# Kernel tuning notes

Hardware: AMD Instinct MI355X
Metric: run time of the kernel (lower is better)

## Reference

```python
import jax, jax.numpy as jnp
import numpy as np


def setup_inputs() -> dict:
    key = jax.random.key(0)
    k1, k2 = jax.random.split(key)
    B, Lc, Lm, D = 8, 2048, 2048, 128
    context = jax.random.normal(k1, (B, Lc, D), dtype=jnp.float32)
    main = jax.random.normal(k2, (B, Lm, D), dtype=jnp.float32)
    return {"context": context, "main": main}


def reference(context, main):
    # weights[b,c,m] = sum_d context[b,c,d] * main[b,m,d]   (Keras dot axes=[2,2])
    weights = jnp.einsum("bcd,bmd->bcm", context, main)
    # K.softmax default axis=-1: normalize over the main-length axis m
    weights = jax.nn.softmax(weights, axis=-1)
    # dot([weights, context], axes=1): contract axis 1 (c) of both -> (B, Lm, D)
    weighted = jnp.einsum("bcm,bcd->bmd", weights, context)
    return main - weighted
```

## Files before the change

### kernel.cpp

```cpp
#include <hip/hip_runtime.h>


#define BATCH 8
#define L_SEQ 2048
#define DD 128
#define SHIFT 40.0f
#define LDA 136
#define ESLD 72

typedef __attribute__((ext_vector_type(8))) short bf16x8;
typedef __attribute__((ext_vector_type(4))) float f32x4;

__device__ __forceinline__ short f2bf(float f) {
    unsigned u = __builtin_bit_cast(unsigned, f);
    return (short)((u + 0x8000u) >> 16);
}

template <int NT>
__device__ __forceinline__ void stage_tile(short* __restrict__ dst,
                                           const float* __restrict__ src,
                                           int nelts, int t) {
    for (int base = 0; base < nelts; base += NT * 8) {
        int flat = base + t * 8;
        const float4* p = (const float4*)(src + flat);
        float4 v0 = p[0];
        float4 v1 = p[1];
        bf16x8 s;
        s[0] = f2bf(v0.x); s[1] = f2bf(v0.y); s[2] = f2bf(v0.z); s[3] = f2bf(v0.w);
        s[4] = f2bf(v1.x); s[5] = f2bf(v1.y); s[6] = f2bf(v1.z); s[7] = f2bf(v1.w);
        int row = flat >> 7;
        int col = flat & 127;
        *(bf16x8*)&dst[row * LDA + col] = s;
    }
}

__global__ __launch_bounds__(256) void zero_kernel(float* __restrict__ p, int n) {
    int i = blockIdx.x * 256 + threadIdx.x;
    if (i < n) p[i] = 0.0f;
}


__global__ __launch_bounds__(256, 4) void stats_kernel(const float* __restrict__ ctx,
                                                       const float* __restrict__ mn,
                                                       float* __restrict__ Lg,
                                                       short* __restrict__ Eg) {
    __shared__ short Cs[64 * LDA];
    __shared__ short Ms[64 * LDA];
    __shared__ short Es[64 * ESLD];

    int bid = blockIdx.x;
    int mc = bid & 3;
    int ct = (bid >> 2) & 31;
    int b  = bid >> 7;
    int t = threadIdx.x;
    int w = t >> 6;
    int l = t & 63;
    int a15 = l & 15;
    int q = l >> 4;

    stage_tile<256>(Cs, ctx + ((size_t)b * L_SEQ + ct * 64) * DD, 64 * DD, t);

    float ls[4] = {0.f, 0.f, 0.f, 0.f};

    for (int mt = 0; mt < 8; ++mt) {
        __syncthreads();
        int m0 = (mc * 8 + mt) * 64;
        stage_tile<256>(Ms, mn + ((size_t)b * L_SEQ + m0) * DD, 64 * DD, t);
        __syncthreads();

        f32x4 sacc[4] = {{0.f,0.f,0.f,0.f},{0.f,0.f,0.f,0.f},{0.f,0.f,0.f,0.f},{0.f,0.f,0.f,0.f}};
        #pragma unroll
        for (int ks = 0; ks < 4; ++ks) {
            int k0 = ks * 32 + q * 8;
            bf16x8 a = *(const bf16x8*)&Ms[(w * 16 + a15) * LDA + k0];
            #pragma unroll
            for (int cg = 0; cg < 4; ++cg) {
                bf16x8 bb = *(const bf16x8*)&Cs[(cg * 16 + a15) * LDA + k0];
                sacc[cg] = __builtin_amdgcn_mfma_f32_16x16x32_bf16(a, bb, sacc[cg], 0, 0, 0);
            }
        }
        #pragma unroll
        for (int cg = 0; cg < 4; ++cg) {
            #pragma unroll
            for (int r = 0; r < 4; ++r) {
                float e = __expf(sacc[cg][r] - SHIFT);
                ls[cg] += e;
                Es[(w * 16 + q * 4 + r) * ESLD + cg * 16 + a15] = f2bf(e);
            }
        }
        __syncthreads();
        #pragma unroll
        for (int i = 0; i < 2; ++i) {
            int flat = i * 2048 + t * 8;
            int m = flat >> 6;
            int c = flat & 63;
            bf16x8 v = *(const bf16x8*)&Es[m * ESLD + c];
            *(bf16x8*)&Eg[((size_t)b * L_SEQ + m0 + m) * L_SEQ + ct * 64 + c] = v;
        }
    }

    #pragma unroll
    for (int cg = 0; cg < 4; ++cg) {
        float v = ls[cg];
        v += __shfl_xor(v, 16);
        v += __shfl_xor(v, 32);
        ls[cg] = v;
    }
    if (l < 16) {
        #pragma unroll
        for (int cg = 0; cg < 4; ++cg)
            atomicAdd(&Lg[(size_t)b * L_SEQ + ct * 64 + cg * 16 + l], ls[cg]);
    }
}

__global__ __launch_bounds__(256) void prep_kernel(const float* __restrict__ ctx,
                                                   const float* __restrict__ Lg,
                                                   short* __restrict__ CtL) {
    __shared__ short Ts[128 * LDA];
    __shared__ float invLs[128];

    int b = blockIdx.x >> 4;
    int cc = blockIdx.x & 15;
    int t = threadIdx.x;

    if (t < 128) invLs[t] = 1.0f / Lg[(size_t)b * L_SEQ + cc * 128 + t];
    __syncthreads();

    const float* src = ctx + ((size_t)b * L_SEQ + cc * 128) * DD;
    #pragma unroll
    for (int i = 0; i < 8; ++i) {
        int flat = i * 2048 + t * 8;
        int r = flat >> 7;
        int c = flat & 127;
        const float4* p = (const float4*)(src + flat);
        float4 v0 = p[0];
        float4 v1 = p[1];
        float il = invLs[r];
        bf16x8 s;
        s[0] = f2bf(v0.x * il); s[1] = f2bf(v0.y * il); s[2] = f2bf(v0.z * il); s[3] = f2bf(v0.w * il);
        s[4] = f2bf(v1.x * il); s[5] = f2bf(v1.y * il); s[6] = f2bf(v1.z * il); s[7] = f2bf(v1.w * il);
        *(bf16x8*)&Ts[r * LDA + c] = s;
    }
    __syncthreads();

    int d = t >> 1;
    int ch = (t & 1) * 64;
    #pragma unroll
    for (int i = 0; i < 8; ++i) {
        int c = ch + i * 8;
        bf16x8 v;
        #pragma unroll
        for (int j = 0; j < 8; ++j) v[j] = Ts[(c + j) * LDA + d];
        *(bf16x8*)&CtL[((size_t)b * DD + d) * L_SEQ + cc * 128 + c] = v;
    }
}

__global__ __launch_bounds__(256, 4) void attend_kernel(const short* __restrict__ Eg,
                                                        const short* __restrict__ CtL,
                                                        const float* __restrict__ mn,
                                                        float* __restrict__ out) {
    __shared__ short Ct[128 * LDA];
    __shared__ short Et[32 * LDA];

    int bid = blockIdx.x;
    int mtile = bid & 63;
    int b = bid >> 6;
    int m0 = mtile * 32;
    int t = threadIdx.x;
    int w = t >> 6;
    int l = t & 63;
    int a15 = l & 15;
    int q = l >> 4;

    f32x4 oacc[2][2] = {{{0.f,0.f,0.f,0.f},{0.f,0.f,0.f,0.f}},
                        {{0.f,0.f,0.f,0.f},{0.f,0.f,0.f,0.f}}};

    for (int cs = 0; cs < 16; ++cs) {
        int c0 = cs * 128;
        __syncthreads();
        #pragma unroll
        for (int i = 0; i < 8; ++i) {
            int flat = i * 2048 + t * 8;
            int d = flat >> 7;
            int c = flat & 127;
            bf16x8 v = *(const bf16x8*)&CtL[((size_t)b * DD + d) * L_SEQ + c0 + c];
            *(bf16x8*)&Ct[d * LDA + c] = v;
        }
        #pragma unroll
        for (int i = 0; i < 2; ++i) {
            int flat = i * 2048 + t * 8;
            int m = flat >> 7;
            int c = flat & 127;
            bf16x8 v = *(const bf16x8*)&Eg[((size_t)b * L_SEQ + m0 + m) * L_SEQ + c0 + c];
            *(bf16x8*)&Et[m * LDA + c] = v;
        }
        __syncthreads();

        #pragma unroll
        for (int ks = 0; ks < 4; ++ks) {
            int k0 = ks * 32 + q * 8;
            bf16x8 a0 = *(const bf16x8*)&Et[a15 * LDA + k0];
            bf16x8 a1 = *(const bf16x8*)&Et[(16 + a15) * LDA + k0];
            #pragma unroll
            for (int g = 0; g < 2; ++g) {
                bf16x8 bb = *(const bf16x8*)&Ct[((w * 2 + g) * 16 + a15) * LDA + k0];
                oacc[0][g] = __builtin_amdgcn_mfma_f32_16x16x32_bf16(a0, bb, oacc[0][g], 0, 0, 0);
                oacc[1][g] = __builtin_amdgcn_mfma_f32_16x16x32_bf16(a1, bb, oacc[1][g], 0, 0, 0);
            }
        }
    }

    #pragma unroll
    for (int mg = 0; mg < 2; ++mg) {
        #pragma unroll
        for (int g = 0; g < 2; ++g) {
            int d = (w * 2 + g) * 16 + a15;
            #pragma unroll
            for (int r = 0; r < 4; ++r) {
                int m = m0 + mg * 16 + q * 4 + r;
                size_t idx = ((size_t)b * L_SEQ + m) * DD + d;
                out[idx] = mn[idx] - oacc[mg][g][r];
            }
        }
    }
}


__global__ __launch_bounds__(256, 4) void stats_fb(const float* __restrict__ ctx,
                                                   const float* __restrict__ mn,
                                                   float* __restrict__ Lg) {
    __shared__ short Cs[64 * LDA];
    __shared__ short Ms[64 * LDA];

    int bid = blockIdx.x;
    int mc = bid & 3;
    int ct = (bid >> 2) & 31;
    int b  = bid >> 7;
    int t = threadIdx.x;
    int w = t >> 6;
    int l = t & 63;
    int a15 = l & 15;
    int q = l >> 4;

    stage_tile<256>(Cs, ctx + ((size_t)b * L_SEQ + ct * 64) * DD, 64 * DD, t);

    float ls[4] = {0.f, 0.f, 0.f, 0.f};
    for (int mt = 0; mt < 8; ++mt) {
        __syncthreads();
        int m0 = (mc * 8 + mt) * 64;
        stage_tile<256>(Ms, mn + ((size_t)b * L_SEQ + m0) * DD, 64 * DD, t);
        __syncthreads();

        f32x4 acc[4] = {{0.f,0.f,0.f,0.f},{0.f,0.f,0.f,0.f},{0.f,0.f,0.f,0.f},{0.f,0.f,0.f,0.f}};
        #pragma unroll
        for (int ks = 0; ks < 4; ++ks) {
            int k0 = ks * 32 + q * 8;
            bf16x8 a = *(const bf16x8*)&Cs[(w * 16 + a15) * LDA + k0];
            #pragma unroll
            for (int g = 0; g < 4; ++g) {
                bf16x8 bb = *(const bf16x8*)&Ms[(g * 16 + a15) * LDA + k0];
                acc[g] = __builtin_amdgcn_mfma_f32_16x16x32_bf16(a, bb, acc[g], 0, 0, 0);
            }
        }
        #pragma unroll
        for (int g = 0; g < 4; ++g)
            #pragma unroll
            for (int r = 0; r < 4; ++r)
                ls[r] += __expf(acc[g][r] - SHIFT);
    }

    #pragma unroll
    for (int r = 0; r < 4; ++r) {
        float v = ls[r];
        v += __shfl_xor(v, 1);
        v += __shfl_xor(v, 2);
        v += __shfl_xor(v, 4);
        v += __shfl_xor(v, 8);
        ls[r] = v;
    }
    if (a15 == 0) {
        int c = ct * 64 + w * 16 + q * 4;
        #pragma unroll
        for (int r = 0; r < 4; ++r)
            atomicAdd(&Lg[(size_t)b * L_SEQ + c + r], ls[r]);
    }
}

__global__ __launch_bounds__(1024, 4) void attend_fb(const float* __restrict__ ctx,
                                                     const float* __restrict__ mn,
                                                     const float* __restrict__ Lg,
                                                     float* __restrict__ out) {
    __shared__ short Mt[64 * LDA];
    __shared__ short Cs[128 * LDA];
    __shared__ short Ct[128 * LDA];
    __shared__ short Ps[64 * LDA];
    __shared__ float invLs[128];

    int bid = blockIdx.x;
    int mtile = bid & 31;
    int b = bid >> 5;
    int m0 = mtile * 64;
    int t = threadIdx.x;
    int w = t >> 6;
    int l = t & 63;
    int a15 = l & 15;
    int q = l >> 4;
    int mg = w & 3;
    int pg = w >> 2;

    stage_tile<1024>(Mt, mn + ((size_t)b * L_SEQ + m0) * DD, 64 * DD, t);

    f32x4 oacc[2] = {{0.f,0.f,0.f,0.f},{0.f,0.f,0.f,0.f}};

    for (int cs = 0; cs < 16; ++cs) {
        int c0 = cs * 128;
        __syncthreads();
        stage_tile<1024>(Cs, ctx + ((size_t)b * L_SEQ + c0) * DD, 128 * DD, t);
        if (t < 128) invLs[t] = 1.0f / Lg[(size_t)b * L_SEQ + c0 + t];
        __syncthreads();

        {
            int cc = t & 127;
            int d0 = (t >> 7) * 16;
            #pragma unroll
            for (int h = 0; h < 2; ++h) {
                bf16x8 v = *(const bf16x8*)&Cs[cc * LDA + d0 + h * 8];
                #pragma unroll
                for (int j = 0; j < 8; ++j)
                    Ct[(d0 + h * 8 + j) * LDA + cc] = v[j];
            }
        }

        f32x4 sacc[2] = {{0.f,0.f,0.f,0.f},{0.f,0.f,0.f,0.f}};
        #pragma unroll
        for (int ks = 0; ks < 4; ++ks) {
            int k0 = ks * 32 + q * 8;
            bf16x8 a = *(const bf16x8*)&Mt[(mg * 16 + a15) * LDA + k0];
            #pragma unroll
            for (int g = 0; g < 2; ++g) {
                bf16x8 bb = *(const bf16x8*)&Cs[((pg * 2 + g) * 16 + a15) * LDA + k0];
                sacc[g] = __builtin_amdgcn_mfma_f32_16x16x32_bf16(a, bb, sacc[g], 0, 0, 0);
            }
        }
        #pragma unroll
        for (int g = 0; g < 2; ++g) {
            int cl = (pg * 2 + g) * 16 + a15;
            float il = invLs[cl];
            #pragma unroll
            for (int r = 0; r < 4; ++r) {
                float p = __expf(sacc[g][r] - SHIFT) * il;
                Ps[(mg * 16 + q * 4 + r) * LDA + cl] = f2bf(p);
            }
        }
        __syncthreads();

        #pragma unroll
        for (int ks = 0; ks < 4; ++ks) {
            int k0 = ks * 32 + q * 8;
            bf16x8 a = *(const bf16x8*)&Ps[(mg * 16 + a15) * LDA + k0];
            #pragma unroll
            for (int g = 0; g < 2; ++g) {
                bf16x8 bb = *(const bf16x8*)&Ct[((pg * 2 + g) * 16 + a15) * LDA + k0];
                oacc[g] = __builtin_amdgcn_mfma_f32_16x16x32_bf16(a, bb, oacc[g], 0, 0, 0);
            }
        }
    }

    #pragma unroll
    for (int g = 0; g < 2; ++g) {
        int dl = (pg * 2 + g) * 16 + a15;
        #pragma unroll
        for (int r = 0; r < 4; ++r) {
            int ml = mg * 16 + q * 4 + r;
            size_t idx = ((size_t)b * L_SEQ + m0 + ml) * DD + dl;
            out[idx] = mn[idx] - oacc[g][r];
        }
    }
}


extern "C" void kernel_launch(void* const* d_in, const int* in_sizes, int n_in,
                              void* d_out, int out_size, void* d_ws, size_t ws_size,
                              hipStream_t stream) {
    const float* ctx = (const float*)d_in[0];
    const float* mn  = (const float*)d_in[1];
    float* out = (float*)d_out;

    const size_t LG_BYTES  = (size_t)BATCH * L_SEQ * sizeof(float);
    const size_t CTL_BYTES = (size_t)BATCH * DD * L_SEQ * sizeof(short);
    const size_t E_BYTES   = (size_t)BATCH * L_SEQ * L_SEQ * sizeof(short);
    const size_t NEED = LG_BYTES + CTL_BYTES + E_BYTES;

    float* Lg = (float*)d_ws;
    int nL = BATCH * L_SEQ;
    zero_kernel<<<(nL + 255) / 256, 256, 0, stream>>>(Lg, nL);

    if (ws_size >= NEED) {
        short* CtL = (short*)((char*)d_ws + LG_BYTES);
        short* Eg  = (short*)((char*)d_ws + LG_BYTES + CTL_BYTES);
        stats_kernel<<<BATCH * 32 * 4, 256, 0, stream>>>(ctx, mn, Lg, Eg);
        prep_kernel<<<BATCH * 16, 256, 0, stream>>>(ctx, Lg, CtL);
        attend_kernel<<<BATCH * 64, 256, 0, stream>>>(Eg, CtL, mn, out);
    } else {
        stats_fb<<<BATCH * 32 * 4, 256, 0, stream>>>(ctx, mn, Lg);
        attend_fb<<<BATCH * 32, 1024, 0, stream>>>(ctx, mn, Lg, out);
    }
}
```

Measured before the change: 127.0 us.

## Pre-convert inputs to swizzled bf16 and stage tiles via direct global-to-LDS loads

Adds a convert kernel that writes context and main as XOR-swizzled bf16 copies and also zeroes the row-sum buffer, which removes the separate zero kernel. The stats and attend kernels then stage tiles with global_load_lds straight into unpadded, swizzled LDS. Attend double-buffers its E and C^T tiles so the next chunk loads while the current one is multiplied. The aim is to cut fp32 conversion work and register round-trips during staging and to hide global latency, at the cost of an extra pass over the inputs, more workspace and lower occupancy.

```diff
diff --git a/kernel.cpp b/kernel.cpp
--- a/kernel.cpp
+++ b/kernel.cpp
@@ -6,14 +6,21 @@
 #define DD 128
 #define SHIFT 40.0f
 #define LDA 136
-#define ESLD 72
+#define ESLD 80
 
 typedef __attribute__((ext_vector_type(8))) short bf16x8;
+typedef __attribute__((ext_vector_type(4))) short bf16x4;
 typedef __attribute__((ext_vector_type(4))) float f32x4;
 
 __device__ __forceinline__ short f2bf(float f) {
     unsigned u = __builtin_bit_cast(unsigned, f);
     return (short)((u + 0x8000u) >> 16);
+}
+
+__device__ __forceinline__ void gl2lds16(const short* g, short* l) {
+    __builtin_amdgcn_global_load_lds(
+        (const __attribute__((address_space(1))) unsigned int*)g,
+        (__attribute__((address_space(3))) unsigned int*)l, 16, 0, 0);
 }
 
 template <int NT>
@@ -40,12 +47,37 @@
 }
 
 
-__global__ __launch_bounds__(256, 4) void stats_kernel(const float* __restrict__ ctx,
-                                                       const float* __restrict__ mn,
+__global__ __launch_bounds__(256) void convert_kernel(const float* __restrict__ ctx,
+                                                      const float* __restrict__ mn,
+                                                      short* __restrict__ Cbf,
+                                                      short* __restrict__ Mbf,
+                                                      float* __restrict__ Lg) {
+    int tid = blockIdx.x * 256 + threadIdx.x;
+    if (tid < BATCH * L_SEQ) Lg[tid] = 0.0f;
+    const int half = BATCH * L_SEQ * DD / 8;
+    int id = tid;
+    const float* src;
+    short* dst;
+    if (id < half) { src = ctx; dst = Cbf; }
+    else           { id -= half; src = mn; dst = Mbf; }
+    int row = id >> 4;
+    int lc = id & 15;
+    const float4* p = (const float4*)(src + ((size_t)row << 7) + lc * 8);
+    float4 v0 = p[0];
+    float4 v1 = p[1];
+    bf16x8 s;
+    s[0] = f2bf(v0.x); s[1] = f2bf(v0.y); s[2] = f2bf(v0.z); s[3] = f2bf(v0.w);
+    s[4] = f2bf(v1.x); s[5] = f2bf(v1.y); s[6] = f2bf(v1.z); s[7] = f2bf(v1.w);
+    int pc = (lc & 8) | ((lc ^ row) & 7);
+    *(bf16x8*)&dst[((size_t)row << 7) + pc * 8] = s;
+}
+
+__global__ __launch_bounds__(256, 3) void stats_kernel(const short* __restrict__ Cbf,
+                                                       const short* __restrict__ Mbf,
                                                        float* __restrict__ Lg,
                                                        short* __restrict__ Eg) {
-    __shared__ short Cs[64 * LDA];
-    __shared__ short Ms[64 * LDA];
+    __shared__ short Cs[64 * 128];
+    __shared__ short Ms[64 * 128];
     __shared__ short Es[64 * ESLD];
 
     int bid = blockIdx.x;
@@ -57,59 +89,82 @@
     int l = t & 63;
     int a15 = l & 15;
     int q = l >> 4;
-
-    stage_tile<256>(Cs, ctx + ((size_t)b * L_SEQ + ct * 64) * DD, 64 * DD, t);
+    int h = a15 & 7;
+
+    {
+        const short* gC = Cbf + ((size_t)(b * L_SEQ + ct * 64)) * DD;
+        const short* gM = Mbf + ((size_t)(b * L_SEQ + mc * 512)) * DD;
+        #pragma unroll
+        for (int ii = 0; ii < 4; ++ii) {
+            int inst = w * 4 + ii;
+            gl2lds16(gC + inst * 512 + l * 8, Cs + inst * 512);
+            gl2lds16(gM + inst * 512 + l * 8, Ms + inst * 512);
+        }
+    }
 
     float ls[4] = {0.f, 0.f, 0.f, 0.f};
 
     for (int mt = 0; mt < 8; ++mt) {
-        __syncthreads();
-        int m0 = (mc * 8 + mt) * 64;
-        stage_tile<256>(Ms, mn + ((size_t)b * L_SEQ + m0) * DD, 64 * DD, t);
+        int m0 = mc * 512 + mt * 64;
         __syncthreads();
 
         f32x4 sacc[4] = {{0.f,0.f,0.f,0.f},{0.f,0.f,0.f,0.f},{0.f,0.f,0.f,0.f},{0.f,0.f,0.f,0.f}};
         #pragma unroll
         for (int ks = 0; ks < 4; ++ks) {
-            int k0 = ks * 32 + q * 8;
-            bf16x8 a = *(const bf16x8*)&Ms[(w * 16 + a15) * LDA + k0];
-            #pragma unroll
-            for (int cg = 0; cg < 4; ++cg) {
-                bf16x8 bb = *(const bf16x8*)&Cs[(cg * 16 + a15) * LDA + k0];
-                sacc[cg] = __builtin_amdgcn_mfma_f32_16x16x32_bf16(a, bb, sacc[cg], 0, 0, 0);
-            }
-        }
-        #pragma unroll
-        for (int cg = 0; cg < 4; ++cg) {
+            int aoff = ((ks * 4 + q) ^ h) * 8;
+            bf16x8 a = *(const bf16x8*)&Cs[(w * 16 + a15) * 128 + aoff];
+            #pragma unroll
+            for (int g = 0; g < 4; ++g) {
+                bf16x8 bb = *(const bf16x8*)&Ms[(g * 16 + a15) * 128 + aoff];
+                sacc[g] = __builtin_amdgcn_mfma_f32_16x16x32_bf16(a, bb, sacc[g], 0, 0, 0);
+            }
+        }
+        #pragma unroll
+        for (int g = 0; g < 4; ++g) {
+            bf16x4 pk;
             #pragma unroll
             for (int r = 0; r < 4; ++r) {
-                float e = __expf(sacc[cg][r] - SHIFT);
-                ls[cg] += e;
-                Es[(w * 16 + q * 4 + r) * ESLD + cg * 16 + a15] = f2bf(e);
-            }
-        }
-        __syncthreads();
+                float e = __expf(sacc[g][r] - SHIFT);
+                ls[r] += e;
+                pk[r] = f2bf(e);
+            }
+            *(bf16x4*)&Es[(g * 16 + a15) * ESLD + w * 16 + q * 4] = pk;
+        }
+        __syncthreads();
+
+        if (mt < 7) {
+            const short* gM = Mbf + ((size_t)(b * L_SEQ + m0 + 64)) * DD;
+            #pragma unroll
+            for (int ii = 0; ii < 4; ++ii) {
+                int inst = w * 4 + ii;
+                gl2lds16(gM + inst * 512 + l * 8, Ms + inst * 512);
+            }
+        }
         #pragma unroll
         for (int i = 0; i < 2; ++i) {
             int flat = i * 2048 + t * 8;
-            int m = flat >> 6;
-            int c = flat & 63;
-            bf16x8 v = *(const bf16x8*)&Es[m * ESLD + c];
-            *(bf16x8*)&Eg[((size_t)b * L_SEQ + m0 + m) * L_SEQ + ct * 64 + c] = v;
-        }
-    }
-
-    #pragma unroll
-    for (int cg = 0; cg < 4; ++cg) {
-        float v = ls[cg];
-        v += __shfl_xor(v, 16);
-        v += __shfl_xor(v, 32);
-        ls[cg] = v;
-    }
-    if (l < 16) {
-        #pragma unroll
-        for (int cg = 0; cg < 4; ++cg)
-            atomicAdd(&Lg[(size_t)b * L_SEQ + ct * 64 + cg * 16 + l], ls[cg]);
+            int ml = flat >> 6;
+            int cl = flat & 63;
+            bf16x8 v = *(const bf16x8*)&Es[ml * ESLD + cl];
+            int pcr = (cl >> 3) ^ (ml & 7);
+            *(bf16x8*)&Eg[((size_t)(b * L_SEQ + m0 + ml)) * L_SEQ + ct * 64 + pcr * 8] = v;
+        }
+    }
+
+    #pragma unroll
+    for (int r = 0; r < 4; ++r) {
+        float v = ls[r];
+        v += __shfl_xor(v, 1);
+        v += __shfl_xor(v, 2);
+        v += __shfl_xor(v, 4);
+        v += __shfl_xor(v, 8);
+        ls[r] = v;
+    }
+    if (a15 == 0) {
+        int c = ct * 64 + w * 16 + q * 4;
+        #pragma unroll
+        for (int r = 0; r < 4; ++r)
+            atomicAdd(&Lg[(size_t)b * L_SEQ + c + r], ls[r]);
     }
 }
 
@@ -126,7 +181,7 @@
     if (t < 128) invLs[t] = 1.0f / Lg[(size_t)b * L_SEQ + cc * 128 + t];
     __syncthreads();
 
-    const float* src = ctx + ((size_t)b * L_SEQ + cc * 128) * DD;
+    const float* src = ctx + ((size_t)(b * L_SEQ + cc * 128)) * DD;
     #pragma unroll
     for (int i = 0; i < 8; ++i) {
         int flat = i * 2048 + t * 8;
@@ -145,22 +200,24 @@
 
     int d = t >> 1;
     int ch = (t & 1) * 64;
+    int key = d & 7;
     #pragma unroll
     for (int i = 0; i < 8; ++i) {
         int c = ch + i * 8;
         bf16x8 v;
         #pragma unroll
         for (int j = 0; j < 8; ++j) v[j] = Ts[(c + j) * LDA + d];
-        *(bf16x8*)&CtL[((size_t)b * DD + d) * L_SEQ + cc * 128 + c] = v;
-    }
-}
-
-__global__ __launch_bounds__(256, 4) void attend_kernel(const short* __restrict__ Eg,
+        int pc = cc * 16 + (ch >> 3) + (i ^ key);
+        *(bf16x8*)&CtL[((size_t)(b * DD + d)) * L_SEQ + pc * 8] = v;
+    }
+}
+
+__global__ __launch_bounds__(256, 2) void attend_kernel(const short* __restrict__ Eg,
                                                         const short* __restrict__ CtL,
                                                         const float* __restrict__ mn,
                                                         float* __restrict__ out) {
-    __shared__ short Ct[128 * LDA];
-    __shared__ short Et[32 * LDA];
+    __shared__ short Et2[2][32 * 128];
+    __shared__ short Ct2[2][128 * 128];
 
     int bid = blockIdx.x;
     int mtile = bid & 63;
@@ -171,42 +228,58 @@
     int l = t & 63;
     int a15 = l & 15;
     int q = l >> 4;
-
-    f32x4 oacc[2][2] = {{{0.f,0.f,0.f,0.f},{0.f,0.f,0.f,0.f}},
-                        {{0.f,0.f,0.f,0.f},{0.f,0.f,0.f,0.f}}};
+    int h = a15 & 7;
+    int lcc = l & 15;
+
+    f32x4 acc[2][2] = {{{0.f,0.f,0.f,0.f},{0.f,0.f,0.f,0.f}},
+                       {{0.f,0.f,0.f,0.f},{0.f,0.f,0.f,0.f}}};
+
+    #pragma unroll
+    for (int ii = 0; ii < 2; ++ii) {
+        int inst = w * 2 + ii;
+        gl2lds16(Eg + ((size_t)(b * L_SEQ + m0 + inst * 4 + q)) * L_SEQ + lcc * 8,
+                 &Et2[0][inst * 512]);
+    }
+    #pragma unroll
+    for (int ii = 0; ii < 8; ++ii) {
+        int inst = w * 8 + ii;
+        gl2lds16(CtL + ((size_t)(b * DD + inst * 4 + q)) * L_SEQ + lcc * 8,
+                 &Ct2[0][inst * 512]);
+    }
 
     for (int cs = 0; cs < 16; ++cs) {
-        int c0 = cs * 128;
-        __syncthreads();
-        #pragma unroll
-        for (int i = 0; i < 8; ++i) {
-            int flat = i * 2048 + t * 8;
-            int d = flat >> 7;
-            int c = flat & 127;
-            bf16x8 v = *(const bf16x8*)&CtL[((size_t)b * DD + d) * L_SEQ + c0 + c];
-            *(bf16x8*)&Ct[d * LDA + c] = v;
-        }
-        #pragma unroll
-        for (int i = 0; i < 2; ++i) {
-            int flat = i * 2048 + t * 8;
-            int m = flat >> 7;
-            int c = flat & 127;
-            bf16x8 v = *(const bf16x8*)&Eg[((size_t)b * L_SEQ + m0 + m) * L_SEQ + c0 + c];
-            *(bf16x8*)&Et[m * LDA + c] = v;
-        }
-        __syncthreads();
-
+        int bp = cs & 1;
+        __syncthreads();
+
+        if (cs < 15) {
+            int c0 = (cs + 1) * 128;
+            #pragma unroll
+            for (int ii = 0; ii < 2; ++ii) {
+                int inst = w * 2 + ii;
+                gl2lds16(Eg + ((size_t)(b * L_SEQ + m0 + inst * 4 + q)) * L_SEQ + c0 + lcc * 8,
+                         &Et2[bp ^ 1][inst * 512]);
+            }
+            #pragma unroll
+            for (int ii = 0; ii < 8; ++ii) {
+                int inst = w * 8 + ii;
+                gl2lds16(CtL + ((size_t)(b * DD + inst * 4 + q)) * L_SEQ + c0 + lcc * 8,
+                         &Ct2[bp ^ 1][inst * 512]);
+            }
+        }
+
+        const short* EtB = Et2[bp];
+        const short* CtB = Ct2[bp];
         #pragma unroll
         for (int ks = 0; ks < 4; ++ks) {
-            int k0 = ks * 32 + q * 8;
-            bf16x8 a0 = *(const bf16x8*)&Et[a15 * LDA + k0];
-            bf16x8 a1 = *(const bf16x8*)&Et[(16 + a15) * LDA + k0];
-            #pragma unroll
-            for (int g = 0; g < 2; ++g) {
-                bf16x8 bb = *(const bf16x8*)&Ct[((w * 2 + g) * 16 + a15) * LDA + k0];
-                oacc[0][g] = __builtin_amdgcn_mfma_f32_16x16x32_bf16(a0, bb, oacc[0][g], 0, 0, 0);
-                oacc[1][g] = __builtin_amdgcn_mfma_f32_16x16x32_bf16(a1, bb, oacc[1][g], 0, 0, 0);
-            }
+            int aoff = ((ks * 4 + q) ^ h) * 8;
+            bf16x8 a0 = *(const bf16x8*)&EtB[a15 * 128 + aoff];
+            bf16x8 a1 = *(const bf16x8*)&EtB[(16 + a15) * 128 + aoff];
+            bf16x8 b0 = *(const bf16x8*)&CtB[((w * 2 + 0) * 16 + a15) * 128 + aoff];
+            bf16x8 b1 = *(const bf16x8*)&CtB[((w * 2 + 1) * 16 + a15) * 128 + aoff];
+            acc[0][0] = __builtin_amdgcn_mfma_f32_16x16x32_bf16(a0, b0, acc[0][0], 0, 0, 0);
+            acc[0][1] = __builtin_amdgcn_mfma_f32_16x16x32_bf16(a0, b1, acc[0][1], 0, 0, 0);
+            acc[1][0] = __builtin_amdgcn_mfma_f32_16x16x32_bf16(a1, b0, acc[1][0], 0, 0, 0);
+            acc[1][1] = __builtin_amdgcn_mfma_f32_16x16x32_bf16(a1, b1, acc[1][1], 0, 0, 0);
         }
     }
 
@@ -218,8 +291,8 @@
             #pragma unroll
             for (int r = 0; r < 4; ++r) {
                 int m = m0 + mg * 16 + q * 4 + r;
-                size_t idx = ((size_t)b * L_SEQ + m) * DD + d;
-                out[idx] = mn[idx] - oacc[mg][g][r];
+                size_t idx = ((size_t)(b * L_SEQ + m)) * DD + d;
+                out[idx] = mn[idx] - acc[mg][g][r];
             }
         }
     }
@@ -323,11 +396,11 @@
             int cc = t & 127;
             int d0 = (t >> 7) * 16;
             #pragma unroll
-            for (int h = 0; h < 2; ++h) {
-                bf16x8 v = *(const bf16x8*)&Cs[cc * LDA + d0 + h * 8];
+            for (int hh = 0; hh < 2; ++hh) {
+                bf16x8 v = *(const bf16x8*)&Cs[cc * LDA + d0 + hh * 8];
                 #pragma unroll
                 for (int j = 0; j < 8; ++j)
-                    Ct[(d0 + h * 8 + j) * LDA + cc] = v[j];
+                    Ct[(d0 + hh * 8 + j) * LDA + cc] = v[j];
             }
         }
 
@@ -386,22 +459,25 @@
     const float* mn  = (const float*)d_in[1];
     float* out = (float*)d_out;
 
-    const size_t LG_BYTES  = (size_t)BATCH * L_SEQ * sizeof(float);
-    const size_t CTL_BYTES = (size_t)BATCH * DD * L_SEQ * sizeof(short);
-    const size_t E_BYTES   = (size_t)BATCH * L_SEQ * L_SEQ * sizeof(short);
-    const size_t NEED = LG_BYTES + CTL_BYTES + E_BYTES;
+    const size_t LG_BYTES = (size_t)BATCH * L_SEQ * sizeof(float);
+    const size_t BF_BYTES = (size_t)BATCH * L_SEQ * DD * sizeof(short);
+    const size_t E_BYTES  = (size_t)BATCH * L_SEQ * L_SEQ * sizeof(short);
+    const size_t NEED = LG_BYTES + 3 * BF_BYTES + E_BYTES;
 
     float* Lg = (float*)d_ws;
-    int nL = BATCH * L_SEQ;
-    zero_kernel<<<(nL + 255) / 256, 256, 0, stream>>>(Lg, nL);
 
     if (ws_size >= NEED) {
-        short* CtL = (short*)((char*)d_ws + LG_BYTES);
-        short* Eg  = (short*)((char*)d_ws + LG_BYTES + CTL_BYTES);
-        stats_kernel<<<BATCH * 32 * 4, 256, 0, stream>>>(ctx, mn, Lg, Eg);
+        short* Cbf = (short*)((char*)d_ws + LG_BYTES);
+        short* Mbf = (short*)((char*)d_ws + LG_BYTES + BF_BYTES);
+        short* CtL = (short*)((char*)d_ws + LG_BYTES + 2 * BF_BYTES);
+        short* Eg  = (short*)((char*)d_ws + LG_BYTES + 3 * BF_BYTES);
+        convert_kernel<<<2048, 256, 0, stream>>>(ctx, mn, Cbf, Mbf, Lg);
+        stats_kernel<<<BATCH * 32 * 4, 256, 0, stream>>>(Cbf, Mbf, Lg, Eg);
         prep_kernel<<<BATCH * 16, 256, 0, stream>>>(ctx, Lg, CtL);
         attend_kernel<<<BATCH * 64, 256, 0, stream>>>(Eg, CtL, mn, out);
     } else {
+        int nL = BATCH * L_SEQ;
+        zero_kernel<<<(nL + 255) / 256, 256, 0, stream>>>(Lg, nL);
         stats_fb<<<BATCH * 32 * 4, 256, 0, stream>>>(ctx, mn, Lg);
         attend_fb<<<BATCH * 32, 1024, 0, stream>>>(ctx, mn, Lg, out);
     }
```

Result: faster. 118.4 us (-6.7%).
